# Optimization experiments

Hardware: AMD Instinct MI355X
Metric: run time of the kernel (lower is better)

The kernel has to match this reference:

```python
import jax, jax.numpy as jnp
import numpy as np

FEATURES = 512
SPLIT_TT = 2
DK = FEATURES // SPLIT_TT           # 256: key width = features // split_tt
NUM_TAPE = 2048                     # ac_config.num_tape_tokens
THRESHOLD = 4.0                     # ac_config.dynamic_tape_length.act_epsilon
TOPK = int(NUM_TAPE // THRESHOLD)   # 512
TOKENS_PER_STEP = 16                # num_token_per_step
BATCH = 64


def setup_inputs() -> dict:
    key = jax.random.key(0)
    kq, kt = jax.random.split(key)
    return {
        "query": jax.random.normal(kq, (BATCH, DK), jnp.float32),
        "halting_prob": jnp.zeros((BATCH,), jnp.float32),
        "remainders": jnp.zeros((BATCH,), jnp.float32),
        "n_updates": jnp.zeros((BATCH,), jnp.float32),
        "score_mask": jnp.zeros((BATCH, NUM_TAPE), jnp.float32),
        "tape_tokens": jax.random.normal(kt, (BATCH, NUM_TAPE, FEATURES), jnp.float32),
    }


def reference(query, halting_prob, remainders, n_updates, score_mask, tape_tokens):
    # One ACT step (take_a_step / act_step) with bank_type='input',
    # act_loss_type='entropy', complex_query=True.
    still_running = (halting_prob < THRESHOLD).astype(jnp.float32)   # [B]

    # keys are the first DK features of the per-example tape bank
    keys = tape_tokens[:, :, :DK]                                    # [B, N, DK]
    scores = jnp.einsum('bd,bnd->bn', query, keys)                   # [B, N]

    # mask already-selected tokens, then top-k
    topk_idx = jax.lax.top_k(scores - score_mask * 1e9, TOPK)[1]     # [B, K] int32

    # NOTE: faithful to original: jnp.take without axis => FLAT gather into
    # scores.ravel(); indices in [0, N) all address row 0 of scores.
    weights = jnp.take(scores, topk_idx)                             # [B, K]
    weights = jax.nn.softmax(weights / (query.shape[-1] ** 0.5), axis=-1)

    entropy = 1.0 - jnp.sum(weights ** 2, axis=-1)                   # [B]
    sum_weights = jnp.sum(weights[:, :TOKENS_PER_STEP], axis=-1)     # [B]

    new_halted = (halting_prob + sum_weights >= THRESHOLD).astype(jnp.float32) * still_running
    still_running = still_running - new_halted
    remainders = remainders + (new_halted + still_running) * entropy
    halting_prob = halting_prob + sum_weights * still_running
    halting_prob = halting_prob + new_halted * (THRESHOLD - halting_prob)
    n_updates = n_updates + still_running + new_halted

    # gather selected tape tokens per example, softmax-weighted merge
    token_sel = jnp.take_along_axis(tape_tokens, topk_idx[..., None], axis=1)  # [B, K, F]
    token_sel = jnp.sum(token_sel * weights[..., None], axis=-2, keepdims=True)  # [B, 1, F]

    # scatter-accumulate selection mask
    score_mask = score_mask + jnp.sum(jax.nn.one_hot(topk_idx, NUM_TAPE), axis=1)  # [B, N]

    # complex_query update
    token_sel_keys = token_sel[:, :, :DK]                            # [B, 1, DK]
    query = (query + jnp.mean(token_sel_keys, axis=1)) / 2.0         # [B, DK]

    return (query, halting_prob, remainders, n_updates, score_mask, token_sel)
```

## Files before the change

### kernel.cpp

```cpp
#include <hip/hip_runtime.h>
#include <math.h>

#define BATCH 64
#define DK 256
#define FEATURES 512
#define NUM_TAPE 2048
#define TOPK 512
#define TOP16 16
#define THRESH 4.0f
#define KCHUNKS 8
#define KPER (TOPK / KCHUNKS)
#define TIECAP 640

#define OFF_Q 0
#define OFF_HP (BATCH * DK)
#define OFF_REM (OFF_HP + BATCH)
#define OFF_NUP (OFF_REM + BATCH)
#define OFF_MASK (OFF_NUP + BATCH)
#define OFF_TSEL (OFF_MASK + BATCH * NUM_TAPE)

#define WS_SCORES 0
#define WS_TOPK 131072
#define WS_WEIGHTS 163840
#define WS_PART 196608

__device__ __forceinline__ unsigned f2key(float f) {
    unsigned u = __float_as_uint(f);
    return (u & 0x80000000u) ? ~u : (u | 0x80000000u);
}

__global__ __launch_bounds__(256) void k_scores(const float* __restrict__ q,
                                                const float* __restrict__ tape,
                                                float* __restrict__ scores) {
    const int b = blockIdx.y;
    const int wave = threadIdx.x >> 6;
    const int lane = threadIdx.x & 63;
    const float4 qf = reinterpret_cast<const float4*>(q + b * DK)[lane];
    const int base = blockIdx.x * 32;
#pragma unroll
    for (int t = 0; t < 8; ++t) {
        const int tok = base + wave + 4 * t;
        const float4 tf =
            reinterpret_cast<const float4*>(tape + ((size_t)b * NUM_TAPE + tok) * FEATURES)[lane];
        float s = qf.x * tf.x + qf.y * tf.y + qf.z * tf.z + qf.w * tf.w;
#pragma unroll
        for (int off = 32; off; off >>= 1) s += __shfl_xor(s, off);
        if (lane == 0) scores[b * NUM_TAPE + tok] = s;
    }
}

__global__ __launch_bounds__(256) void k_topk(const float* __restrict__ scores,
                                              const float* __restrict__ mask_in,
                                              const float* __restrict__ hp_in,
                                              const float* __restrict__ rem_in,
                                              const float* __restrict__ nup_in,
                                              int* __restrict__ topk_ws,
                                              float* __restrict__ weights_ws,
                                              float* __restrict__ out) {
    const int b = blockIdx.x;
    const int tid = threadIdx.x;
    __shared__ int hist[256];
    __shared__ int sh_digit, sh_hi;
    __shared__ int sel_idx[TOPK];
    __shared__ unsigned sel_key[TOPK];
    __shared__ float sel_w[TOPK];
    __shared__ float red[256];
    __shared__ int tie_idx[TIECAP];
    __shared__ int tie_cnt, sel_cnt;
    __shared__ int in16_idx[TOP16];

    unsigned key[8];
#pragma unroll
    for (int i = 0; i < 8; ++i) {
        const int e = i * 256 + tid;
        const float v = scores[b * NUM_TAPE + e] - mask_in[b * NUM_TAPE + e] * 1e9f;
        key[i] = f2key(v);
    }

    unsigned T512 = 0, T16 = 0;
    int krem512 = 0, krem16 = 0;
    for (int sel = 0; sel < 2; ++sel) {
        const int k = sel ? TOP16 : TOPK;
        unsigned prefix = 0;
        int krem = k;
        for (int p = 0; p < 4; ++p) {
            const int shift = 24 - 8 * p;
            hist[tid] = 0;
            __syncthreads();
#pragma unroll
            for (int i = 0; i < 8; ++i) {
                const unsigned kk = key[i];
                const bool act = (p == 0) || ((kk >> (shift + 8)) == (prefix >> (shift + 8)));
                if (act) atomicAdd(&hist[(kk >> shift) & 0xFF], 1);
            }
            __syncthreads();
            for (int off = 1; off < 256; off <<= 1) {
                const int v = (tid + off < 256) ? hist[tid + off] : 0;
                __syncthreads();
                hist[tid] += v;
                __syncthreads();
            }
            const int sv = hist[tid];
            const int nxt = (tid < 255) ? hist[tid + 1] : 0;
            if (sv >= krem && nxt < krem) {
                sh_digit = tid;
                sh_hi = nxt;
            }
            __syncthreads();
            prefix |= ((unsigned)sh_digit) << shift;
            krem -= sh_hi;
            __syncthreads();
        }
        if (sel == 0) {
            T512 = prefix;
            krem512 = krem;
        } else {
            T16 = prefix;
            krem16 = krem;
        }
    }

    if (tid == 0) {
        sel_cnt = 0;
        tie_cnt = 0;
    }
    __syncthreads();
#pragma unroll
    for (int i = 0; i < 8; ++i) {
        const int e = i * 256 + tid;
        const unsigned kk = key[i];
        if (kk > T512) {
            const int p = atomicAdd(&sel_cnt, 1);
            sel_idx[p] = e;
            sel_key[p] = kk;
        } else if (kk == T512) {
            const int p = atomicAdd(&tie_cnt, 1);
            if (p < TIECAP) tie_idx[p] = e;
        }
    }
    __syncthreads();
    int tc = tie_cnt < TIECAP ? tie_cnt : TIECAP;
    for (int t = tid; t < tc; t += 256) {
        const int my = tie_idx[t];
        int rank = 0;
        for (int u = 0; u < tc; ++u) rank += (tie_idx[u] < my);
        if (rank < krem512) {
            const int p = atomicAdd(&sel_cnt, 1);
            sel_idx[p] = my;
            sel_key[p] = T512;
        }
    }
    __syncthreads();

    if (tid == 0) tie_cnt = 0;
    __syncthreads();
#pragma unroll
    for (int i = 0; i < 8; ++i) {
        const int e = i * 256 + tid;
        if (key[i] == T16) {
            const int p = atomicAdd(&tie_cnt, 1);
            if (p < TIECAP) tie_idx[p] = e;
        }
    }
    __syncthreads();
    tc = tie_cnt < TIECAP ? tie_cnt : TIECAP;
    for (int t = tid; t < tc; t += 256) {
        const int my = tie_idx[t];
        int rank = 0;
        for (int u = 0; u < tc; ++u) rank += (tie_idx[u] < my);
        if (rank < krem16) in16_idx[rank] = my;
    }
    __syncthreads();

    float m = -1e30f;
    for (int s = tid; s < TOPK; s += 256) {
        const float w = scores[sel_idx[s]] * 0.0625f;
        sel_w[s] = w;
        m = fmaxf(m, w);
    }
    red[tid] = m;
    __syncthreads();
    for (int s = 128; s; s >>= 1) {
        if (tid < s) red[tid] = fmaxf(red[tid], red[tid + s]);
        __syncthreads();
    }
    const float mmax = red[0];
    __syncthreads();

    float lsum = 0.f;
    for (int s = tid; s < TOPK; s += 256) {
        const float w = expf(sel_w[s] - mmax);
        sel_w[s] = w;
        lsum += w;
    }
    red[tid] = lsum;
    __syncthreads();
    for (int s = 128; s; s >>= 1) {
        if (tid < s) red[tid] += red[tid + s];
        __syncthreads();
    }
    const float inv = 1.0f / red[0];
    __syncthreads();

    float lsq = 0.f, l16 = 0.f;
    for (int s = tid; s < TOPK; s += 256) {
        const float w = sel_w[s] * inv;
        const int idx = sel_idx[s];
        weights_ws[b * TOPK + s] = w;
        topk_ws[b * TOPK + s] = idx;
        lsq += w * w;
        const unsigned kk = sel_key[s];
        bool in16 = (kk > T16);
        if (kk == T16) {
            for (int u = 0; u < krem16; ++u)
                if (in16_idx[u] == idx) in16 = true;
        }
        if (in16) l16 += w;
    }
    red[tid] = lsq;
    __syncthreads();
    for (int s = 128; s; s >>= 1) {
        if (tid < s) red[tid] += red[tid + s];
        __syncthreads();
    }
    const float sumsq = red[0];
    __syncthreads();
    red[tid] = l16;
    __syncthreads();
    for (int s = 128; s; s >>= 1) {
        if (tid < s) red[tid] += red[tid + s];
        __syncthreads();
    }
    const float s16 = red[0];
    __syncthreads();

    if (tid == 0) {
        const float hp = hp_in[b], rem = rem_in[b], nup = nup_in[b];
        const float entropy = 1.0f - sumsq;
        const float still = (hp < THRESH) ? 1.f : 0.f;
        const float nh = ((hp + s16) >= THRESH ? 1.f : 0.f) * still;
        const float st2 = still - nh;
        out[OFF_REM + b] = rem + (nh + st2) * entropy;
        float hp1 = hp + s16 * st2;
        hp1 = hp1 + nh * (THRESH - hp1);
        out[OFF_HP + b] = hp1;
        out[OFF_NUP + b] = nup + st2 + nh;
    }

    for (int n = tid; n < NUM_TAPE; n += 256)
        out[OFF_MASK + b * NUM_TAPE + n] = mask_in[b * NUM_TAPE + n];
    __syncthreads();
    for (int s = tid; s < TOPK; s += 256) {
        const int idx = sel_idx[s];
        out[OFF_MASK + b * NUM_TAPE + idx] = mask_in[b * NUM_TAPE + idx] + 1.0f;
    }
}

__global__ __launch_bounds__(512) void k_gather(const float* __restrict__ tape,
                                                const int* __restrict__ topk_ws,
                                                const float* __restrict__ weights_ws,
                                                float* __restrict__ partials) {
    const int b = blockIdx.y;
    const int kc = blockIdx.x;
    const int f = threadIdx.x;
    __shared__ float wsh[KPER];
    __shared__ int ish[KPER];
    if (f < KPER) {
        wsh[f] = weights_ws[b * TOPK + kc * KPER + f];
        ish[f] = topk_ws[b * TOPK + kc * KPER + f];
    }
    __syncthreads();
    float acc = 0.f;
#pragma unroll 4
    for (int k = 0; k < KPER; ++k) {
        acc = fmaf(wsh[k], tape[((size_t)b * NUM_TAPE + ish[k]) * FEATURES + f], acc);
    }
    partials[((size_t)b * KCHUNKS + kc) * FEATURES + f] = acc;
}

__global__ __launch_bounds__(512) void k_finish(const float* __restrict__ q,
                                                const float* __restrict__ partials,
                                                float* __restrict__ out) {
    const int b = blockIdx.x;
    const int f = threadIdx.x;
    float s = 0.f;
#pragma unroll
    for (int kc = 0; kc < KCHUNKS; ++kc) s += partials[((size_t)b * KCHUNKS + kc) * FEATURES + f];
    out[OFF_TSEL + b * FEATURES + f] = s;
    if (f < DK) out[OFF_Q + b * DK + f] = (q[b * DK + f] + s) * 0.5f;
}

extern "C" void kernel_launch(void* const* d_in, const int* in_sizes, int n_in,
                              void* d_out, int out_size, void* d_ws, size_t ws_size,
                              hipStream_t stream) {
    const float* q = (const float*)d_in[0];
    const float* hp = (const float*)d_in[1];
    const float* rem = (const float*)d_in[2];
    const float* nup = (const float*)d_in[3];
    const float* mask = (const float*)d_in[4];
    const float* tape = (const float*)d_in[5];
    float* out = (float*)d_out;
    float* ws = (float*)d_ws;

    float* scores = ws + WS_SCORES;
    int* topk = (int*)(ws + WS_TOPK);
    float* weights = ws + WS_WEIGHTS;
    float* partials = ws + WS_PART;

    k_scores<<<dim3(NUM_TAPE / 32, BATCH), 256, 0, stream>>>(q, tape, scores);
    k_topk<<<BATCH, 256, 0, stream>>>(scores, mask, hp, rem, nup, topk, weights, out);
    k_gather<<<dim3(KCHUNKS, BATCH), 512, 0, stream>>>(tape, topk, weights, partials);
    k_finish<<<BATCH, 512, 0, stream>>>(q, partials, out);
}
```

Measured before the change: 55.99 us.

## Restructure top-k radix select with wave scans and vectorize gather and finish

The top-k kernel now runs 512 threads, each holding four keys loaded as float4. The 256-bin prefix scan uses wave shuffles plus per-wave totals instead of a barrier-heavy shared-memory scan. The top-16 threshold is found by a second radix select over only the 512 already-selected keys rather than all 2048. Softmax and the entropy reductions become one element per thread with shuffle reductions, and the mask copy uses float4. The gather and finish kernels switch to float4 loads with four row-slices per block reduced in shared memory, which adds some shared-memory traffic and barriers.

```diff
diff --git a/kernel.cpp b/kernel.cpp
--- a/kernel.cpp
+++ b/kernel.cpp
@@ -49,7 +49,7 @@
     }
 }
 
-__global__ __launch_bounds__(256) void k_topk(const float* __restrict__ scores,
+__global__ __launch_bounds__(512) void k_topk(const float* __restrict__ scores,
                                               const float* __restrict__ mask_in,
                                               const float* __restrict__ hp_in,
                                               const float* __restrict__ rem_in,
@@ -59,66 +59,68 @@
                                               float* __restrict__ out) {
     const int b = blockIdx.x;
     const int tid = threadIdx.x;
+    const int lane = tid & 63;
+    const int wv = tid >> 6;
     __shared__ int hist[256];
+    __shared__ int chunkTot[4];
     __shared__ int sh_digit, sh_hi;
     __shared__ int sel_idx[TOPK];
     __shared__ unsigned sel_key[TOPK];
-    __shared__ float sel_w[TOPK];
-    __shared__ float red[256];
+    __shared__ float redf[8];
     __shared__ int tie_idx[TIECAP];
     __shared__ int tie_cnt, sel_cnt;
     __shared__ int in16_idx[TOP16];
 
-    unsigned key[8];
-#pragma unroll
-    for (int i = 0; i < 8; ++i) {
-        const int e = i * 256 + tid;
-        const float v = scores[b * NUM_TAPE + e] - mask_in[b * NUM_TAPE + e] * 1e9f;
-        key[i] = f2key(v);
-    }
-
-    unsigned T512 = 0, T16 = 0;
-    int krem512 = 0, krem16 = 0;
-    for (int sel = 0; sel < 2; ++sel) {
-        const int k = sel ? TOP16 : TOPK;
-        unsigned prefix = 0;
-        int krem = k;
-        for (int p = 0; p < 4; ++p) {
-            const int shift = 24 - 8 * p;
-            hist[tid] = 0;
-            __syncthreads();
-#pragma unroll
-            for (int i = 0; i < 8; ++i) {
-                const unsigned kk = key[i];
-                const bool act = (p == 0) || ((kk >> (shift + 8)) == (prefix >> (shift + 8)));
-                if (act) atomicAdd(&hist[(kk >> shift) & 0xFF], 1);
+    const float4 sc = reinterpret_cast<const float4*>(scores + (size_t)b * NUM_TAPE)[tid];
+    const float4 mk = reinterpret_cast<const float4*>(mask_in + (size_t)b * NUM_TAPE)[tid];
+    unsigned key[4];
+    key[0] = f2key(sc.x - mk.x * 1e9f);
+    key[1] = f2key(sc.y - mk.y * 1e9f);
+    key[2] = f2key(sc.z - mk.z * 1e9f);
+    key[3] = f2key(sc.w - mk.w * 1e9f);
+
+    unsigned prefix = 0;
+    int krem = TOPK;
+#pragma unroll
+    for (int p = 0; p < 4; ++p) {
+        const int shift = 24 - 8 * p;
+        if (tid < 256) hist[tid] = 0;
+        __syncthreads();
+#pragma unroll
+        for (int i = 0; i < 4; ++i) {
+            const unsigned kk = key[i];
+            const bool act = (p == 0) || ((kk >> (shift + 8)) == (prefix >> (shift + 8)));
+            if (act) atomicAdd(&hist[(kk >> shift) & 0xFF], 1);
+        }
+        __syncthreads();
+        int v = 0, hcnt = 0;
+        if (tid < 256) {
+            hcnt = hist[tid];
+            v = hcnt;
+#pragma unroll
+            for (int off = 1; off < 64; off <<= 1) {
+                const int t = __shfl_down(v, off);
+                if (lane + off < 64) v += t;
             }
-            __syncthreads();
-            for (int off = 1; off < 256; off <<= 1) {
-                const int v = (tid + off < 256) ? hist[tid + off] : 0;
-                __syncthreads();
-                hist[tid] += v;
-                __syncthreads();
+            if (lane == 0) chunkTot[wv] = v;
+        }
+        __syncthreads();
+        if (tid < 256) {
+#pragma unroll
+            for (int w2 = 0; w2 < 4; ++w2)
+                if (w2 > wv) v += chunkTot[w2];
+            if (v >= krem && (v - hcnt) < krem) {
+                sh_digit = tid;
+                sh_hi = v - hcnt;
             }
-            const int sv = hist[tid];
-            const int nxt = (tid < 255) ? hist[tid + 1] : 0;
-            if (sv >= krem && nxt < krem) {
-                sh_digit = tid;
-                sh_hi = nxt;
-            }
-            __syncthreads();
-            prefix |= ((unsigned)sh_digit) << shift;
-            krem -= sh_hi;
-            __syncthreads();
-        }
-        if (sel == 0) {
-            T512 = prefix;
-            krem512 = krem;
-        } else {
-            T16 = prefix;
-            krem16 = krem;
-        }
-    }
+        }
+        __syncthreads();
+        prefix |= ((unsigned)sh_digit) << shift;
+        krem -= sh_hi;
+        __syncthreads();
+    }
+    const unsigned T512 = prefix;
+    const int krem512 = krem;
 
     if (tid == 0) {
         sel_cnt = 0;
@@ -126,8 +128,8 @@
     }
     __syncthreads();
 #pragma unroll
-    for (int i = 0; i < 8; ++i) {
-        const int e = i * 256 + tid;
+    for (int i = 0; i < 4; ++i) {
+        const int e = 4 * tid + i;
         const unsigned kk = key[i];
         if (kk > T512) {
             const int p = atomicAdd(&sel_cnt, 1);
@@ -140,7 +142,7 @@
     }
     __syncthreads();
     int tc = tie_cnt < TIECAP ? tie_cnt : TIECAP;
-    for (int t = tid; t < tc; t += 256) {
+    for (int t = tid; t < tc; t += 512) {
         const int my = tie_idx[t];
         int rank = 0;
         for (int u = 0; u < tc; ++u) rank += (tie_idx[u] < my);
@@ -152,19 +154,57 @@
     }
     __syncthreads();
 
+    const unsigned kk2 = sel_key[tid];
+    prefix = 0;
+    krem = TOP16;
+#pragma unroll
+    for (int p = 0; p < 4; ++p) {
+        const int shift = 24 - 8 * p;
+        if (tid < 256) hist[tid] = 0;
+        __syncthreads();
+        {
+            const bool act = (p == 0) || ((kk2 >> (shift + 8)) == (prefix >> (shift + 8)));
+            if (act) atomicAdd(&hist[(kk2 >> shift) & 0xFF], 1);
+        }
+        __syncthreads();
+        int v = 0, hcnt = 0;
+        if (tid < 256) {
+            hcnt = hist[tid];
+            v = hcnt;
+#pragma unroll
+            for (int off = 1; off < 64; off <<= 1) {
+                const int t = __shfl_down(v, off);
+                if (lane + off < 64) v += t;
+            }
+            if (lane == 0) chunkTot[wv] = v;
+        }
+        __syncthreads();
+        if (tid < 256) {
+#pragma unroll
+            for (int w2 = 0; w2 < 4; ++w2)
+                if (w2 > wv) v += chunkTot[w2];
+            if (v >= krem && (v - hcnt) < krem) {
+                sh_digit = tid;
+                sh_hi = v - hcnt;
+            }
+        }
+        __syncthreads();
+        prefix |= ((unsigned)sh_digit) << shift;
+        krem -= sh_hi;
+        __syncthreads();
+    }
+    const unsigned T16 = prefix;
+    const int krem16 = krem;
+
     if (tid == 0) tie_cnt = 0;
     __syncthreads();
-#pragma unroll
-    for (int i = 0; i < 8; ++i) {
-        const int e = i * 256 + tid;
-        if (key[i] == T16) {
-            const int p = atomicAdd(&tie_cnt, 1);
-            if (p < TIECAP) tie_idx[p] = e;
-        }
+    if (kk2 == T16) {
+        const int p = atomicAdd(&tie_cnt, 1);
+        if (p < TIECAP) tie_idx[p] = sel_idx[tid];
     }
     __syncthreads();
     tc = tie_cnt < TIECAP ? tie_cnt : TIECAP;
-    for (int t = tid; t < tc; t += 256) {
+    for (int t = tid; t < tc; t += 512) {
         const int my = tie_idx[t];
         int rank = 0;
         for (int u = 0; u < tc; ++u) rank += (tie_idx[u] < my);
@@ -172,67 +212,56 @@
     }
     __syncthreads();
 
-    float m = -1e30f;
-    for (int s = tid; s < TOPK; s += 256) {
-        const float w = scores[sel_idx[s]] * 0.0625f;
-        sel_w[s] = w;
-        m = fmaxf(m, w);
-    }
-    red[tid] = m;
-    __syncthreads();
-    for (int s = 128; s; s >>= 1) {
-        if (tid < s) red[tid] = fmaxf(red[tid], red[tid + s]);
-        __syncthreads();
-    }
-    const float mmax = red[0];
-    __syncthreads();
-
-    float lsum = 0.f;
-    for (int s = tid; s < TOPK; s += 256) {
-        const float w = expf(sel_w[s] - mmax);
-        sel_w[s] = w;
-        lsum += w;
-    }
-    red[tid] = lsum;
-    __syncthreads();
-    for (int s = 128; s; s >>= 1) {
-        if (tid < s) red[tid] += red[tid + s];
-        __syncthreads();
-    }
-    const float inv = 1.0f / red[0];
-    __syncthreads();
-
-    float lsq = 0.f, l16 = 0.f;
-    for (int s = tid; s < TOPK; s += 256) {
-        const float w = sel_w[s] * inv;
-        const int idx = sel_idx[s];
-        weights_ws[b * TOPK + s] = w;
-        topk_ws[b * TOPK + s] = idx;
-        lsq += w * w;
-        const unsigned kk = sel_key[s];
-        bool in16 = (kk > T16);
-        if (kk == T16) {
-            for (int u = 0; u < krem16; ++u)
-                if (in16_idx[u] == idx) in16 = true;
-        }
-        if (in16) l16 += w;
-    }
-    red[tid] = lsq;
-    __syncthreads();
-    for (int s = 128; s; s >>= 1) {
-        if (tid < s) red[tid] += red[tid + s];
-        __syncthreads();
-    }
-    const float sumsq = red[0];
-    __syncthreads();
-    red[tid] = l16;
-    __syncthreads();
-    for (int s = 128; s; s >>= 1) {
-        if (tid < s) red[tid] += red[tid + s];
-        __syncthreads();
-    }
-    const float s16 = red[0];
-    __syncthreads();
+    const int myidx = sel_idx[tid];
+    const float wraw = scores[myidx] * 0.0625f;
+
+    float m = wraw;
+#pragma unroll
+    for (int off = 32; off; off >>= 1) m = fmaxf(m, __shfl_xor(m, off));
+    if (lane == 0) redf[wv] = m;
+    __syncthreads();
+#pragma unroll
+    for (int w2 = 0; w2 < 8; ++w2) m = fmaxf(m, redf[w2]);
+    __syncthreads();
+
+    const float e = expf(wraw - m);
+    float s = e;
+#pragma unroll
+    for (int off = 32; off; off >>= 1) s += __shfl_xor(s, off);
+    if (lane == 0) redf[wv] = s;
+    __syncthreads();
+    s = 0.f;
+#pragma unroll
+    for (int w2 = 0; w2 < 8; ++w2) s += redf[w2];
+    __syncthreads();
+
+    const float w = e / s;
+    weights_ws[b * TOPK + tid] = w;
+    topk_ws[b * TOPK + tid] = myidx;
+
+    float lsq = w * w;
+#pragma unroll
+    for (int off = 32; off; off >>= 1) lsq += __shfl_xor(lsq, off);
+    if (lane == 0) redf[wv] = lsq;
+    __syncthreads();
+    float sumsq = 0.f;
+#pragma unroll
+    for (int w2 = 0; w2 < 8; ++w2) sumsq += redf[w2];
+    __syncthreads();
+
+    bool in16 = (kk2 > T16);
+    if (kk2 == T16) {
+        for (int u = 0; u < krem16; ++u)
+            if (in16_idx[u] == myidx) in16 = true;
+    }
+    float l16 = in16 ? w : 0.f;
+#pragma unroll
+    for (int off = 32; off; off >>= 1) l16 += __shfl_xor(l16, off);
+    if (lane == 0) redf[wv] = l16;
+    __syncthreads();
+    float s16 = 0.f;
+#pragma unroll
+    for (int w2 = 0; w2 < 8; ++w2) s16 += redf[w2];
 
     if (tid == 0) {
         const float hp = hp_in[b], rem = rem_in[b], nup = nup_in[b];
@@ -247,13 +276,9 @@
         out[OFF_NUP + b] = nup + st2 + nh;
     }
 
-    for (int n = tid; n < NUM_TAPE; n += 256)
-        out[OFF_MASK + b * NUM_TAPE + n] = mask_in[b * NUM_TAPE + n];
-    __syncthreads();
-    for (int s = tid; s < TOPK; s += 256) {
-        const int idx = sel_idx[s];
-        out[OFF_MASK + b * NUM_TAPE + idx] = mask_in[b * NUM_TAPE + idx] + 1.0f;
-    }
+    reinterpret_cast<float4*>(out + OFF_MASK + (size_t)b * NUM_TAPE)[tid] = mk;
+    __syncthreads();
+    out[OFF_MASK + b * NUM_TAPE + myidx] = mask_in[b * NUM_TAPE + myidx] + 1.0f;
 }
 
 __global__ __launch_bounds__(512) void k_gather(const float* __restrict__ tape,
@@ -262,32 +287,81 @@
                                                 float* __restrict__ partials) {
     const int b = blockIdx.y;
     const int kc = blockIdx.x;
-    const int f = threadIdx.x;
+    const int rs = threadIdx.x >> 7;
+    const int f4 = threadIdx.x & 127;
     __shared__ float wsh[KPER];
     __shared__ int ish[KPER];
-    if (f < KPER) {
-        wsh[f] = weights_ws[b * TOPK + kc * KPER + f];
-        ish[f] = topk_ws[b * TOPK + kc * KPER + f];
-    }
-    __syncthreads();
-    float acc = 0.f;
+    __shared__ float4 shacc[512];
+    if (threadIdx.x < KPER) {
+        wsh[threadIdx.x] = weights_ws[b * TOPK + kc * KPER + threadIdx.x];
+        ish[threadIdx.x] = topk_ws[b * TOPK + kc * KPER + threadIdx.x];
+    }
+    __syncthreads();
+    float4 acc = {0.f, 0.f, 0.f, 0.f};
 #pragma unroll 4
-    for (int k = 0; k < KPER; ++k) {
-        acc = fmaf(wsh[k], tape[((size_t)b * NUM_TAPE + ish[k]) * FEATURES + f], acc);
-    }
-    partials[((size_t)b * KCHUNKS + kc) * FEATURES + f] = acc;
+    for (int k = rs; k < KPER; k += 4) {
+        const float w = wsh[k];
+        const float4 t =
+            reinterpret_cast<const float4*>(tape + ((size_t)b * NUM_TAPE + ish[k]) * FEATURES)[f4];
+        acc.x = fmaf(w, t.x, acc.x);
+        acc.y = fmaf(w, t.y, acc.y);
+        acc.z = fmaf(w, t.z, acc.z);
+        acc.w = fmaf(w, t.w, acc.w);
+    }
+    shacc[threadIdx.x] = acc;
+    __syncthreads();
+    if (threadIdx.x < 128) {
+        const float4 a0 = shacc[f4];
+        const float4 a1 = shacc[128 + f4];
+        const float4 a2 = shacc[256 + f4];
+        const float4 a3 = shacc[384 + f4];
+        float4 r;
+        r.x = (a0.x + a1.x) + (a2.x + a3.x);
+        r.y = (a0.y + a1.y) + (a2.y + a3.y);
+        r.z = (a0.z + a1.z) + (a2.z + a3.z);
+        r.w = (a0.w + a1.w) + (a2.w + a3.w);
+        reinterpret_cast<float4*>(partials + ((size_t)b * KCHUNKS + kc) * FEATURES)[f4] = r;
+    }
 }
 
 __global__ __launch_bounds__(512) void k_finish(const float* __restrict__ q,
                                                 const float* __restrict__ partials,
                                                 float* __restrict__ out) {
     const int b = blockIdx.x;
-    const int f = threadIdx.x;
-    float s = 0.f;
-#pragma unroll
-    for (int kc = 0; kc < KCHUNKS; ++kc) s += partials[((size_t)b * KCHUNKS + kc) * FEATURES + f];
-    out[OFF_TSEL + b * FEATURES + f] = s;
-    if (f < DK) out[OFF_Q + b * DK + f] = (q[b * DK + f] + s) * 0.5f;
+    const int g = threadIdx.x >> 7;
+    const int f4 = threadIdx.x & 127;
+    __shared__ float4 sh[512];
+    const float4* pp = reinterpret_cast<const float4*>(partials + (size_t)b * KCHUNKS * FEATURES);
+    const float4 a = pp[g * 128 + f4];
+    const float4 c = pp[(g + 4) * 128 + f4];
+    float4 r;
+    r.x = a.x + c.x;
+    r.y = a.y + c.y;
+    r.z = a.z + c.z;
+    r.w = a.w + c.w;
+    sh[threadIdx.x] = r;
+    __syncthreads();
+    if (threadIdx.x < 128) {
+        const float4 s0 = sh[f4];
+        const float4 s1 = sh[128 + f4];
+        const float4 s2 = sh[256 + f4];
+        const float4 s3 = sh[384 + f4];
+        float4 s;
+        s.x = (s0.x + s1.x) + (s2.x + s3.x);
+        s.y = (s0.y + s1.y) + (s2.y + s3.y);
+        s.z = (s0.z + s1.z) + (s2.z + s3.z);
+        s.w = (s0.w + s1.w) + (s2.w + s3.w);
+        reinterpret_cast<float4*>(out + OFF_TSEL + (size_t)b * FEATURES)[f4] = s;
+        if (f4 < 64) {
+            const float4 qv = reinterpret_cast<const float4*>(q + (size_t)b * DK)[f4];
+            float4 nq;
+            nq.x = (qv.x + s.x) * 0.5f;
+            nq.y = (qv.y + s.y) * 0.5f;
+            nq.z = (qv.z + s.z) * 0.5f;
+            nq.w = (qv.w + s.w) * 0.5f;
+            reinterpret_cast<float4*>(out + OFF_Q + (size_t)b * DK)[f4] = nq;
+        }
+    }
 }
 
 extern "C" void kernel_launch(void* const* d_in, const int* in_sizes, int n_in,
@@ -308,7 +382,7 @@
     float* partials = ws + WS_PART;
 
     k_scores<<<dim3(NUM_TAPE / 32, BATCH), 256, 0, stream>>>(q, tape, scores);
-    k_topk<<<BATCH, 256, 0, stream>>>(scores, mask, hp, rem, nup, topk, weights, out);
+    k_topk<<<BATCH, 512, 0, stream>>>(scores, mask, hp, rem, nup, topk, weights, out);
     k_gather<<<dim3(KCHUNKS, BATCH), 512, 0, stream>>>(tape, topk, weights, partials);
     k_finish<<<BATCH, 512, 0, stream>>>(q, partials, out);
 }
```

Result: faster. 50.73 us, median of 2 (-9.4%).
